# Optimization experiments

Measured on AMD Instinct MI355X. Metric: run time of the kernel, lower is better.

The kernel has to match this reference:

```python
import jax, jax.numpy as jnp
import numpy as np

N_FFT = 1024
HOP_LENGTH = 480
NB_MAX_FRAMES = 1000
N_MELS = 64
SPEC_WIDTH = 1024
N_BINS = N_FFT // 2 + 1  # 513


def setup_inputs() -> dict:
    key = jax.random.key(0)
    B, L = 32, 480000  # 10 s @ 48 kHz -> 1001 frames, truncated to 1000
    waveform = jax.random.normal(key, (B, L), dtype=jnp.float32)

    # DFT-as-conv weights, exactly as in the torch module (hann periodic window)
    n = np.arange(N_FFT, dtype=np.float32)
    window = 0.5 - 0.5 * np.cos(2.0 * np.pi * n / N_FFT)  # torch.hann_window (periodic)
    k = np.arange(N_BINS, dtype=np.float32)[:, None]
    angle = 2.0 * np.pi * k * n[None, :] / N_FFT
    stft_weights = np.concatenate(
        [window * np.cos(angle), -window * np.sin(angle)], axis=0
    ).astype(np.float32)  # [2*N_BINS, N_FFT]

    # Stand-in for HF's slaney mel filterbank (513 -> 64): non-negative, sparse-ish scale
    mel_filters = jax.random.uniform(
        jax.random.fold_in(key, 1), (N_BINS, N_MELS), dtype=jnp.float32
    ) * 0.02

    return {
        "waveform": waveform,
        "stft_weights": jnp.asarray(stft_weights),
        "mel_filters": mel_filters,
    }


def _bilinear_align_corners(img, out_h, out_w):
    """F.interpolate(mode='bilinear', align_corners=True) on [B,C,H,W]."""
    B, C, H, W = img.shape

    def coords(out, inn):
        scale = (inn - 1) / max(out - 1, 1)
        pos = jnp.arange(out, dtype=jnp.float32) * scale
        i0 = jnp.clip(jnp.floor(pos).astype(jnp.int32), 0, inn - 1)
        return i0, pos - i0.astype(jnp.float32)

    h0, hw = coords(out_h, H)
    w0, ww = coords(out_w, W)
    h1 = jnp.minimum(h0 + 1, H - 1)
    w1 = jnp.minimum(w0 + 1, W - 1)

    rows = (img[:, :, h0, :] * (1.0 - hw)[None, None, :, None]
            + img[:, :, h1, :] * hw[None, None, :, None])  # [B,C,out_h,W]
    out = rows[..., w0] * (1.0 - ww) + rows[..., w1] * ww   # [B,C,out_h,out_w]
    return out


def reference(waveform, stft_weights, mel_filters):
    pad = N_FFT // 2
    x = jnp.pad(waveform, ((0, 0), (pad, pad)), mode="reflect")  # center=True

    # strided conv1d == frame extraction + GEMM with the DFT matrix
    T = (x.shape[1] - N_FFT) // HOP_LENGTH + 1
    idx = jnp.arange(T)[:, None] * HOP_LENGTH + jnp.arange(N_FFT)[None, :]
    frames = x[:, idx]                                   # [B, T, N_FFT]
    spec = jnp.einsum("btn,kn->bkt", frames, stft_weights)  # [B, 2*N_BINS, T]

    real = spec[:, :N_BINS, :]
    imag = spec[:, N_BINS:, :]
    power = (real * real + imag * imag)[:, :, :NB_MAX_FRAMES]  # [B, 513, 1000]

    mel = jnp.einsum("bft,fm->bmt", power, mel_filters)        # [B, 64, 1000]
    log_mel = 10.0 * jnp.log10(jnp.clip(mel, 1e-10))

    img = jnp.transpose(log_mel, (0, 2, 1))[:, None]           # [B, 1, 1000, 64]
    return _bilinear_align_corners(img, SPEC_WIDTH, N_MELS)    # [B, 1, 1024, 64]
```

## Files before the change

kernel.cpp:

```cpp
#include <hip/hip_runtime.h>
#include <hip/hip_bf16.h>
#include <math.h>

#define LWAV   480000
#define XHALF  240512
#define NBATCH 32
#define TOUT   1000
#define NMEL   64
#define PSTR   576
#define SPECW  1024

#define XPE_OFF  0u
#define XPO_OFF  15392768u
#define WEO_OFF  30785536u
#define WMT_OFF  31834112u
#define PW_OFF   31907840u
#define LM_OFF   68771840u
#define W256_OFF 76963840u

typedef __attribute__((ext_vector_type(8))) __bf16 bf16x8;
typedef __attribute__((ext_vector_type(8))) unsigned short ushort8;
typedef __attribute__((ext_vector_type(4))) float  f32x4;

__device__ __forceinline__ void gload16(const void* g, void* l) {
  __builtin_amdgcn_global_load_lds((const __attribute__((address_space(1))) void*)g,
                                   (__attribute__((address_space(3))) void*)l, 16, 0, 0);
}
#define WAIT_VM(n)  asm volatile("s_waitcnt vmcnt(" #n ")" ::: "memory")
#define BAR() __builtin_amdgcn_s_barrier()

__device__ __forceinline__ float bf2f(unsigned short u) {
  return __uint_as_float((unsigned)u << 16);
}

#define NG1 (NBATCH * (XHALF / 8))
#define NG2 ((1024 * 512) / 8)
#define NG3 ((NMEL * PSTR) / 8)
#define NG4 (1024 / 8)

__global__ void prep_kernel(const float* __restrict__ wav,
                            const float* __restrict__ wstft,
                            const float* __restrict__ mf,
                            unsigned char* __restrict__ ws) {
  __hip_bfloat16* xpE = (__hip_bfloat16*)(ws + XPE_OFF);
  __hip_bfloat16* xpO = (__hip_bfloat16*)(ws + XPO_OFF);
  __hip_bfloat16* weo = (__hip_bfloat16*)(ws + WEO_OFF);
  __hip_bfloat16* wmt = (__hip_bfloat16*)(ws + WMT_OFF);
  __hip_bfloat16* w256 = (__hip_bfloat16*)(ws + W256_OFF);
  int idx = blockIdx.x * blockDim.x + threadIdx.x;
  if (idx < NG1) {
    int b = idx / (XHALF / 8);
    int g = idx - b * (XHALF / 8);
    const float* src = wav + (size_t)b * LWAV;
    __hip_bfloat16 e[8], o[8];
    if (g >= 32 && g <= 30030) {
      const float4* p = (const float4*)(src + 16 * g - 512);
#pragma unroll
      for (int u = 0; u < 4; ++u) {
        float4 v = p[u];
        e[2 * u]     = __float2bfloat16(v.x);
        o[2 * u]     = __float2bfloat16(v.y);
        e[2 * u + 1] = __float2bfloat16(v.z);
        o[2 * u + 1] = __float2bfloat16(v.w);
      }
    } else {
      for (int i = 0; i < 16; ++i) {
        int q = 16 * g + i;
        int s = q - 512;
        if (s < 0) s = -s;
        else if (s >= LWAV) s = 2 * (LWAV - 1) - s;
        __hip_bfloat16 v = __float2bfloat16(src[s]);
        if (i & 1) o[i >> 1] = v; else e[i >> 1] = v;
      }
    }
    *(uint4*)(xpE + (size_t)b * XHALF + 8 * g) = *(const uint4*)e;
    *(uint4*)(xpO + (size_t)b * XHALF + 8 * g) = *(const uint4*)o;
  } else if (idx < NG1 + NG2) {
    int v = idx - NG1;
    int row = v >> 6;
    int mseg = (v & 63) * 8;
    int comp = row >> 8, j = row & 255;
    __hip_bfloat16 t[8];
    if (comp < 2) {
      const float4* srow = (const float4*)(wstft + (size_t)(comp == 0 ? j : 513 + j) * 1024 + 2 * mseg);
#pragma unroll
      for (int u = 0; u < 4; ++u) {
        float4 vv = srow[u];
        t[2 * u]     = __float2bfloat16(vv.x);
        t[2 * u + 1] = __float2bfloat16(vv.z);
      }
    } else {
      const float4* w0 = (const float4*)(wstft + 2 * mseg);
#pragma unroll
      for (int u = 0; u < 4; ++u) {
        float4 wwv = w0[u];
        float wo[2] = {wwv.y, wwv.w};
#pragma unroll
        for (int h = 0; h < 2; ++h) {
          int mm = mseg + 2 * u + h;
          int q = (j * mm) & 511;
          float ang = (float)q * 0.012271846f;
          float val = (comp == 2) ? wo[h] * cosf(ang) : -wo[h] * sinf(ang);
          t[2 * u + h] = __float2bfloat16(val);
        }
      }
    }
    *(uint4*)(weo + (size_t)row * 512 + mseg) = *(const uint4*)t;
  } else if (idx < NG1 + NG2 + NG3) {
    int j = idx - NG1 - NG2;
    int n = j / (PSTR / 8);
    int k0 = (j - n * (PSTR / 8)) * 8;
    for (int k = k0; k < k0 + 8; ++k)
      wmt[n * PSTR + k] = __float2bfloat16(k < 513 ? mf[k * NMEL + n] : 0.0f);
  } else if (idx < NG1 + NG2 + NG3 + NG4) {
    int j = idx - NG1 - NG2 - NG3;
    int part = j >> 6;
    int m0 = (j & 63) * 8;
    __hip_bfloat16 t[8];
#pragma unroll
    for (int h = 0; h < 8; ++h) {
      int m = m0 + h;
      float v = part == 0 ? wstft[(size_t)256 * 1024 + 2 * m]
                          : wstft[(size_t)769 * 1024 + 2 * m + 1];
      t[h] = __float2bfloat16(v);
    }
    *(uint4*)(w256 + part * 512 + m0) = *(const uint4*)t;
  }
}

__launch_bounds__(256, 2)
__global__ void p256_kernel(unsigned char* __restrict__ ws) {
  __hip_bfloat16* pw = (__hip_bfloat16*)(ws + PW_OFF);
  const int tid  = threadIdx.x;
  const int l16  = tid & 15;
  const int fidx = blockIdx.x * 16 + (tid >> 4);
  const int b = fidx / 1000, t = fidx - b * 1000;

  const unsigned short* xe = (const unsigned short*)(ws + XPE_OFF) +
      (size_t)b * XHALF + 240 * (size_t)t + l16 * 32;
  const unsigned short* xo = (const unsigned short*)(ws + XPO_OFF) +
      (size_t)b * XHALF + 240 * (size_t)t + l16 * 32;
  const unsigned short* we = (const unsigned short*)(ws + W256_OFF) + l16 * 32;
  const unsigned short* wo = (const unsigned short*)(ws + W256_OFF) + 512 + l16 * 32;

  ushort8 ev[4], ov[4], wev[4], wov[4];
#pragma unroll
  for (int q = 0; q < 4; ++q) {
    ev[q]  = *(const ushort8*)(xe + q * 8);
    ov[q]  = *(const ushort8*)(xo + q * 8);
    wev[q] = *(const ushort8*)(we + q * 8);
    wov[q] = *(const ushort8*)(wo + q * 8);
  }
  float dc = 0.f, ds = 0.f;
#pragma unroll
  for (int q = 0; q < 4; ++q)
#pragma unroll
    for (int u = 0; u < 8; ++u) {
      dc += bf2f(ev[q][u]) * bf2f(wev[q][u]);
      ds += bf2f(ov[q][u]) * bf2f(wov[q][u]);
    }
#pragma unroll
  for (int d = 1; d < 16; d <<= 1) {
    dc += __shfl_xor(dc, d);
    ds += __shfl_xor(ds, d);
  }
  if (l16 == 0)
    pw[((size_t)b * TOUT + t) * PSTR + 256] = __float2bfloat16(dc * dc + ds * ds);
}

#define STFT_NWG 500
__launch_bounds__(512, 1)
__global__ void stft_kernel(unsigned char* __restrict__ ws) {
  __shared__ __align__(16) unsigned char lds[147456];
  __hip_bfloat16* pw = (__hip_bfloat16*)(ws + PW_OFF);

  const int tid  = threadIdx.x;
  const int lane = tid & 63;
  const int w    = tid >> 6;
  const int wm   = w >> 2;
  const int wc   = w & 3;

  const int orig = blockIdx.x;
  const int q8 = STFT_NWG / 8, r8 = STFT_NWG % 8;
  const int xcd = orig & 7;
  const int wg = (xcd < r8 ? xcd * (q8 + 1) : r8 * (q8 + 1) + (xcd - r8) * q8) + (orig >> 3);
  const int j0 = (wg & 3) * 64;
  const int m0 = (wg >> 2) * 256;

  const unsigned char* gsA[4];
  const unsigned char* gsB[2];
#pragma unroll
  for (int i = 0; i < 4; ++i) {
    int r = (w * 4 + i) * 8 + (lane >> 3);
    int q = lane & 7;
    int l1 = q ^ (r & 7);
    int m = m0 + r;
    int bb = m / 1000, tt = m - bb * 1000;
    size_t fbase = ((size_t)bb * XHALF + 240 * (size_t)tt) * 2;
    gsA[i] = (l1 < 4) ? (ws + XPE_OFF + fbase + l1 * 16)
                      : (ws + XPO_OFF + fbase + (l1 - 4) * 16);
  }
#pragma unroll
  for (int i = 0; i < 2; ++i) {
    int r = (w * 2 + i) * 16 + (lane >> 2);
    int q = lane & 3;
    int l2 = q ^ ((r >> 1) & 3);
    int comp = (r >> 4) & 3;
    int jv = j0 + (r >> 6) * 16 + (r & 15);
    gsB[i] = ws + WEO_OFF + ((size_t)(comp * 256 + jv) * 512) * 2 + l2 * 16;
  }

#define STG(c, kt) do {                                                          \
    gload16(gsA[0] + (size_t)(kt) * 64, lds + (c) * 49152 + (w * 4 + 0) * 1024); \
    gload16(gsA[1] + (size_t)(kt) * 64, lds + (c) * 49152 + (w * 4 + 1) * 1024); \
    gload16(gsA[2] + (size_t)(kt) * 64, lds + (c) * 49152 + (w * 4 + 2) * 1024); \
    gload16(gsA[3] + (size_t)(kt) * 64, lds + (c) * 49152 + (w * 4 + 3) * 1024); \
    gload16(gsB[0] + (size_t)(kt) * 64, lds + (c) * 49152 + 32768 + (w * 2 + 0) * 1024); \
    gload16(gsB[1] + (size_t)(kt) * 64, lds + (c) * 49152 + 32768 + (w * 2 + 1) * 1024); \
  } while (0)

  const int l15 = lane & 15, lc = lane >> 4;
  const int swA = (lc ^ (l15 & 7)) << 4;
  const unsigned char* aeB = lds + (wm * 128 + l15) * 128 + swA;
  const unsigned char* aoB = lds + (wm * 128 + l15) * 128 + (swA ^ 64);
  const int swB = (lc ^ ((l15 >> 1) & 3)) << 4;
  const unsigned char* bB = lds + 32768 + (wc * 64 + l15) * 64 + swB;

  bf16x8 ae[8], ao[8], bfr[4];
  f32x4 acc[8][4];
#pragma unroll
  for (int a = 0; a < 8; ++a)
#pragma unroll
    for (int b2 = 0; b2 < 4; ++b2) acc[a][b2] = (f32x4){0.f, 0.f, 0.f, 0.f};

  STG(0, 0);
  STG(1, 1);
  WAIT_VM(6);
  BAR();

#pragma unroll
  for (int kt = 0; kt < 16; ++kt) {
    const int cur = kt % 3;
    if (kt + 2 < 16) STG((kt + 2) % 3, kt + 2);
#pragma unroll
    for (int mf = 0; mf < 8; ++mf)
      ae[mf] = *(const bf16x8*)(aeB + cur * 49152 + mf * 2048);
#pragma unroll
    for (int nf = 0; nf < 4; ++nf)
      bfr[nf] = *(const bf16x8*)(bB + cur * 49152 + nf * 1024);
    __builtin_amdgcn_s_setprio(1);
#pragma unroll
    for (int mf = 0; mf < 8; ++mf) {
      acc[mf][0] = __builtin_amdgcn_mfma_f32_16x16x32_bf16(ae[mf], bfr[0], acc[mf][0], 0, 0, 0);
      acc[mf][1] = __builtin_amdgcn_mfma_f32_16x16x32_bf16(ae[mf], bfr[1], acc[mf][1], 0, 0, 0);
    }
    __builtin_amdgcn_s_setprio(0);
#pragma unroll
    for (int mf = 0; mf < 8; ++mf)
      ao[mf] = *(const bf16x8*)(aoB + cur * 49152 + mf * 2048);
    __builtin_amdgcn_s_setprio(1);
#pragma unroll
    for (int mf = 0; mf < 8; ++mf) {
      acc[mf][2] = __builtin_amdgcn_mfma_f32_16x16x32_bf16(ao[mf], bfr[2], acc[mf][2], 0, 0, 0);
      acc[mf][3] = __builtin_amdgcn_mfma_f32_16x16x32_bf16(ao[mf], bfr[3], acc[mf][3], 0, 0, 0);
    }
    __builtin_amdgcn_s_setprio(0);
    if (kt < 14) { WAIT_VM(6); BAR(); }
    else if (kt == 14) { WAIT_VM(0); BAR(); }
  }

  const int j = j0 + wc * 16 + l15;
  const float th = (float)j * 0.0061359233f;
  const float ct = cosf(th), st = sinf(th);
#pragma unroll
  for (int mf = 0; mf < 8; ++mf)
#pragma unroll
    for (int r = 0; r < 4; ++r) {
      int m = m0 + wm * 128 + mf * 16 + lc * 4 + r;
      float Ec = acc[mf][0][r], Es = acc[mf][1][r];
      float Oc = acc[mf][2][r], Os = acc[mf][3][r];
      float tOc = ct * Oc + st * Os;
      float tOs = ct * Os - st * Oc;
      float re1 = Ec + tOc, im1 = Es + tOs;
      float re2 = Ec - tOc, im2 = Es - tOs;
      pw[(size_t)m * PSTR + j]         = __float2bfloat16(re1 * re1 + im1 * im1);
      pw[(size_t)m * PSTR + (512 - j)] = __float2bfloat16(re2 * re2 + im2 * im2);
    }
}

__launch_bounds__(256, 4)
__global__ void mel_kernel(unsigned char* __restrict__ ws) {
  __shared__ __align__(16) unsigned char sA[64 * 128];
  __shared__ __align__(16) unsigned char sBt[64 * 128];
  const unsigned char* pwb  = ws + PW_OFF;
  const unsigned char* wmtb = ws + WMT_OFF;
  float* lm = (float*)(ws + LM_OFF);

  const int tid = threadIdx.x;
  const int lane = tid & 63;
  const int wid  = tid >> 6;
  const int m0 = blockIdx.x * 64;

  const int strow = tid >> 3;
  const int scol  = (tid & 7) << 4;

  const unsigned char* aptr[2];
  const unsigned char* bptr[2];
  unsigned char* aldst[2];
  unsigned char* bldst[2];
#pragma unroll
  for (int jj = 0; jj < 2; ++jj) {
    int rr = jj * 32 + strow;
    aptr[jj] = pwb + (size_t)(m0 + rr) * (PSTR * 2) + (scol ^ ((rr & 7) << 4));
    bptr[jj] = wmtb + (size_t)rr * (PSTR * 2) + (scol ^ ((rr & 7) << 4));
    aldst[jj] = &sA [jj * 4096 + wid * 1024];
    bldst[jj] = &sBt[jj * 4096 + wid * 1024];
  }

  f32x4 acc[4];
#pragma unroll
  for (int fr = 0; fr < 4; ++fr) acc[fr] = (f32x4){0.f, 0.f, 0.f, 0.f};

  for (int kk = 0; kk < PSTR; kk += 64) {
    __syncthreads();
#pragma unroll
    for (int jj = 0; jj < 2; ++jj) gload16(aptr[jj] + (size_t)kk * 2, aldst[jj]);
#pragma unroll
    for (int jj = 0; jj < 2; ++jj) gload16(bptr[jj] + (size_t)kk * 2, bldst[jj]);
    __syncthreads();
#pragma unroll
    for (int ks = 0; ks < 2; ++ks) {
      const int kby = ks * 64 + ((lane >> 4) << 4);
      bf16x8 af, bfr[4];
      {
        int rr = wid * 16 + (lane & 15);
        af = *(const bf16x8*)&sA[rr * 128 + (kby ^ ((rr & 7) << 4))];
      }
#pragma unroll
      for (int fr = 0; fr < 4; ++fr) {
        int rr = fr * 16 + (lane & 15);
        bfr[fr] = *(const bf16x8*)&sBt[rr * 128 + (kby ^ ((rr & 7) << 4))];
      }
#pragma unroll
      for (int fr = 0; fr < 4; ++fr)
        acc[fr] = __builtin_amdgcn_mfma_f32_16x16x32_bf16(af, bfr[fr], acc[fr], 0, 0, 0);
    }
  }

  const int col = lane & 15;
  const int rg  = lane >> 4;
#pragma unroll
  for (int fr = 0; fr < 4; ++fr) {
    int n = fr * 16 + col;
#pragma unroll
    for (int rr = 0; rr < 4; ++rr) {
      int mrow = wid * 16 + rg * 4 + rr;
      float v = acc[fr][rr];
      lm[(size_t)(m0 + mrow) * NMEL + n] = 10.0f * log10f(fmaxf(v, 1e-10f));
    }
  }
}

__global__ void interp_kernel(const unsigned char* __restrict__ ws, float* __restrict__ out) {
  const float* lm = (const float*)(ws + LM_OFF);
  int idx = blockIdx.x * blockDim.x + threadIdx.x;
  if (idx >= NBATCH * SPECW * 16) return;
  int m4 = idx & 15;
  int h  = (idx >> 4) & (SPECW - 1);
  int b  = idx >> 14;
  const float scale = (float)(999.0 / 1023.0);
  float pos = (float)h * scale;
  int i0 = (int)floorf(pos);
  if (i0 > TOUT - 1) i0 = TOUT - 1;
  float wgt = pos - (float)i0;
  int i1 = i0 + 1;
  if (i1 > TOUT - 1) i1 = TOUT - 1;
  const float4* r0 = (const float4*)(lm + ((size_t)b * TOUT + i0) * NMEL);
  const float4* r1 = (const float4*)(lm + ((size_t)b * TOUT + i1) * NMEL);
  float4 a = r0[m4], c = r1[m4];
  float4 o;
  o.x = a.x * (1.0f - wgt) + c.x * wgt;
  o.y = a.y * (1.0f - wgt) + c.y * wgt;
  o.z = a.z * (1.0f - wgt) + c.z * wgt;
  o.w = a.w * (1.0f - wgt) + c.w * wgt;
  ((float4*)out)[idx] = o;
}

extern "C" void kernel_launch(void* const* d_in, const int* in_sizes, int n_in,
                              void* d_out, int out_size, void* d_ws, size_t ws_size,
                              hipStream_t stream) {
  (void)in_sizes; (void)n_in; (void)out_size; (void)ws_size;
  const float* wav   = (const float*)d_in[0];
  const float* wstft = (const float*)d_in[1];
  const float* mf    = (const float*)d_in[2];
  unsigned char* ws  = (unsigned char*)d_ws;
  float* out = (float*)d_out;

  const int tot = NG1 + NG2 + NG3 + NG4;
  prep_kernel<<<(tot + 255) / 256, 256, 0, stream>>>(wav, wstft, mf, ws);
  stft_kernel<<<STFT_NWG, 512, 0, stream>>>(ws);
  p256_kernel<<<2000, 256, 0, stream>>>(ws);
  mel_kernel<<<500, 256, 0, stream>>>(ws);
  interp_kernel<<<(NBATCH * SPECW * 16) / 256, 256, 0, stream>>>(ws, out);
}
```

Before: 90.69 us.

## Retile STFT GEMM to 128x256 blocks with double buffering and two blocks per CU

```diff
diff --git a/kernel.cpp b/kernel.cpp
--- a/kernel.cpp
+++ b/kernel.cpp
@@ -27,6 +27,7 @@
                                    (__attribute__((address_space(3))) void*)l, 16, 0, 0);
 }
 #define WAIT_VM(n)  asm volatile("s_waitcnt vmcnt(" #n ")" ::: "memory")
+#define WAIT_LGKM0  asm volatile("s_waitcnt lgkmcnt(0)" ::: "memory")
 #define BAR() __builtin_amdgcn_s_barrier()
 
 __device__ __forceinline__ float bf2f(unsigned short u) {
@@ -168,124 +169,141 @@
     pw[((size_t)b * TOUT + t) * PSTR + 256] = __float2bfloat16(dc * dc + ds * ds);
 }
 
-#define STFT_NWG 500
-__launch_bounds__(512, 1)
+#define STFT_NWG 1000
+__launch_bounds__(256, 2)
 __global__ void stft_kernel(unsigned char* __restrict__ ws) {
-  __shared__ __align__(16) unsigned char lds[147456];
+  __shared__ __align__(16) unsigned char lds[65536];
   __hip_bfloat16* pw = (__hip_bfloat16*)(ws + PW_OFF);
 
   const int tid  = threadIdx.x;
   const int lane = tid & 63;
   const int w    = tid >> 6;
-  const int wm   = w >> 2;
-  const int wc   = w & 3;
+  const int wm   = w >> 1;
+  const int wn   = w & 1;
 
   const int orig = blockIdx.x;
-  const int q8 = STFT_NWG / 8, r8 = STFT_NWG % 8;
-  const int xcd = orig & 7;
-  const int wg = (xcd < r8 ? xcd * (q8 + 1) : r8 * (q8 + 1) + (xcd - r8) * q8) + (orig >> 3);
+  const int wg = (orig & 7) * 125 + (orig >> 3);
   const int j0 = (wg & 3) * 64;
-  const int m0 = (wg >> 2) * 256;
+  const int m0 = (wg >> 2) * 128;
 
   const unsigned char* gsA[4];
-  const unsigned char* gsB[2];
-#pragma unroll
-  for (int i = 0; i < 4; ++i) {
-    int r = (w * 4 + i) * 8 + (lane >> 3);
-    int q = lane & 7;
-    int l1 = q ^ (r & 7);
-    int m = m0 + r;
-    int bb = m / 1000, tt = m - bb * 1000;
-    size_t fbase = ((size_t)bb * XHALF + 240 * (size_t)tt) * 2;
-    gsA[i] = (l1 < 4) ? (ws + XPE_OFF + fbase + l1 * 16)
-                      : (ws + XPO_OFF + fbase + (l1 - 4) * 16);
-  }
-#pragma unroll
-  for (int i = 0; i < 2; ++i) {
-    int r = (w * 2 + i) * 16 + (lane >> 2);
-    int q = lane & 3;
-    int l2 = q ^ ((r >> 1) & 3);
-    int comp = (r >> 4) & 3;
-    int jv = j0 + (r >> 6) * 16 + (r & 15);
-    gsB[i] = ws + WEO_OFF + ((size_t)(comp * 256 + jv) * 512) * 2 + l2 * 16;
-  }
-
-#define STG(c, kt) do {                                                          \
-    gload16(gsA[0] + (size_t)(kt) * 64, lds + (c) * 49152 + (w * 4 + 0) * 1024); \
-    gload16(gsA[1] + (size_t)(kt) * 64, lds + (c) * 49152 + (w * 4 + 1) * 1024); \
-    gload16(gsA[2] + (size_t)(kt) * 64, lds + (c) * 49152 + (w * 4 + 2) * 1024); \
-    gload16(gsA[3] + (size_t)(kt) * 64, lds + (c) * 49152 + (w * 4 + 3) * 1024); \
-    gload16(gsB[0] + (size_t)(kt) * 64, lds + (c) * 49152 + 32768 + (w * 2 + 0) * 1024); \
-    gload16(gsB[1] + (size_t)(kt) * 64, lds + (c) * 49152 + 32768 + (w * 2 + 1) * 1024); \
+  {
+    int sl  = tid & 7;
+    int rq  = tid >> 3;
+    int slp = sl ^ (rq & 7);
+#pragma unroll
+    for (int i = 0; i < 4; ++i) {
+      int row = i * 32 + rq;
+      int m = m0 + row;
+      int bb = m / 1000, tt = m - bb * 1000;
+      size_t fb = ((size_t)bb * XHALF + 240 * (size_t)tt) * 2;
+      gsA[i] = (slp < 4) ? (ws + XPE_OFF + fb + slp * 16)
+                         : (ws + XPO_OFF + fb + (slp - 4) * 16);
+    }
+  }
+  const unsigned char* gsB[4];
+  {
+    int sl2  = tid & 3;
+    int rq2  = tid >> 2;
+    int sl2p = sl2 ^ (rq2 & 3);
+#pragma unroll
+    for (int i = 0; i < 4; ++i) {
+      int row2 = i * 64 + rq2;
+      int comp = (row2 >> 4) & 3;
+      int jj = j0 + (row2 >> 6) * 16 + (row2 & 15);
+      gsB[i] = ws + WEO_OFF + (size_t)(comp * 256 + jj) * 1024 + sl2p * 16;
+    }
+  }
+
+#define STG(c, kt) do {                                                           \
+    gload16(gsA[0] + (size_t)(kt) * 64, lds + (c) * 32768 + 0 * 4096 + w * 1024); \
+    gload16(gsA[1] + (size_t)(kt) * 64, lds + (c) * 32768 + 1 * 4096 + w * 1024); \
+    gload16(gsA[2] + (size_t)(kt) * 64, lds + (c) * 32768 + 2 * 4096 + w * 1024); \
+    gload16(gsA[3] + (size_t)(kt) * 64, lds + (c) * 32768 + 3 * 4096 + w * 1024); \
+    gload16(gsB[0] + (size_t)(kt) * 64, lds + (c) * 32768 + 16384 + 0 * 4096 + w * 1024); \
+    gload16(gsB[1] + (size_t)(kt) * 64, lds + (c) * 32768 + 16384 + 1 * 4096 + w * 1024); \
+    gload16(gsB[2] + (size_t)(kt) * 64, lds + (c) * 32768 + 16384 + 2 * 4096 + w * 1024); \
+    gload16(gsB[3] + (size_t)(kt) * 64, lds + (c) * 32768 + 16384 + 3 * 4096 + w * 1024); \
   } while (0)
 
   const int l15 = lane & 15, lc = lane >> 4;
-  const int swA = (lc ^ (l15 & 7)) << 4;
-  const unsigned char* aeB = lds + (wm * 128 + l15) * 128 + swA;
-  const unsigned char* aoB = lds + (wm * 128 + l15) * 128 + (swA ^ 64);
-  const int swB = (lc ^ ((l15 >> 1) & 3)) << 4;
-  const unsigned char* bB = lds + 32768 + (wc * 64 + l15) * 64 + swB;
-
-  bf16x8 ae[8], ao[8], bfr[4];
-  f32x4 acc[8][4];
-#pragma unroll
-  for (int a = 0; a < 8; ++a)
-#pragma unroll
-    for (int b2 = 0; b2 < 4; ++b2) acc[a][b2] = (f32x4){0.f, 0.f, 0.f, 0.f};
+  const int aoffs = (wm * 64 + l15) * 128 + ((lc ^ (l15 & 7)) << 4);
+  const int boffs = 16384 + (wn * 128 + l15) * 64 + ((lc ^ (l15 & 3)) << 4);
+
+  bf16x8 ae[4], ao[4], bfr[8];
+  f32x4 acc[4][8];
+#pragma unroll
+  for (int a = 0; a < 4; ++a)
+#pragma unroll
+    for (int b2 = 0; b2 < 8; ++b2) acc[a][b2] = (f32x4){0.f, 0.f, 0.f, 0.f};
+
+#define RD_ALL(C) do {                                                       \
+    _Pragma("unroll")                                                        \
+    for (int mf = 0; mf < 4; ++mf) {                                         \
+      ae[mf] = *(const bf16x8*)(lds + (C) + aoffs + mf * 2048);              \
+      ao[mf] = *(const bf16x8*)(lds + (C) + (aoffs ^ 64) + mf * 2048);       \
+    }                                                                        \
+    _Pragma("unroll")                                                        \
+    for (int nf = 0; nf < 8; ++nf)                                           \
+      bfr[nf] = *(const bf16x8*)(lds + (C) + boffs + nf * 1024);             \
+  } while (0)
+
+#define MFMA_ALL() do {                                                      \
+    __builtin_amdgcn_s_setprio(1);                                           \
+    _Pragma("unroll")                                                        \
+    for (int mf = 0; mf < 4; ++mf)                                           \
+      _Pragma("unroll")                                                      \
+      for (int g = 0; g < 2; ++g) {                                          \
+        acc[mf][g*4+0] = __builtin_amdgcn_mfma_f32_16x16x32_bf16(            \
+            ae[mf], bfr[g*4+0], acc[mf][g*4+0], 0, 0, 0);                    \
+        acc[mf][g*4+1] = __builtin_amdgcn_mfma_f32_16x16x32_bf16(            \
+            ae[mf], bfr[g*4+1], acc[mf][g*4+1], 0, 0, 0);                    \
+        acc[mf][g*4+2] = __builtin_amdgcn_mfma_f32_16x16x32_bf16(            \
+            ao[mf], bfr[g*4+2], acc[mf][g*4+2], 0, 0, 0);                    \
+        acc[mf][g*4+3] = __builtin_amdgcn_mfma_f32_16x16x32_bf16(            \
+            ao[mf], bfr[g*4+3], acc[mf][g*4+3], 0, 0, 0);                    \
+      }                                                                      \
+    __builtin_amdgcn_s_setprio(0);                                           \
+  } while (0)
 
   STG(0, 0);
   STG(1, 1);
-  WAIT_VM(6);
+  WAIT_VM(8);
   BAR();
 
 #pragma unroll
   for (int kt = 0; kt < 16; ++kt) {
-    const int cur = kt % 3;
-    if (kt + 2 < 16) STG((kt + 2) % 3, kt + 2);
-#pragma unroll
-    for (int mf = 0; mf < 8; ++mf)
-      ae[mf] = *(const bf16x8*)(aeB + cur * 49152 + mf * 2048);
-#pragma unroll
-    for (int nf = 0; nf < 4; ++nf)
-      bfr[nf] = *(const bf16x8*)(bB + cur * 49152 + nf * 1024);
-    __builtin_amdgcn_s_setprio(1);
-#pragma unroll
-    for (int mf = 0; mf < 8; ++mf) {
-      acc[mf][0] = __builtin_amdgcn_mfma_f32_16x16x32_bf16(ae[mf], bfr[0], acc[mf][0], 0, 0, 0);
-      acc[mf][1] = __builtin_amdgcn_mfma_f32_16x16x32_bf16(ae[mf], bfr[1], acc[mf][1], 0, 0, 0);
-    }
-    __builtin_amdgcn_s_setprio(0);
-#pragma unroll
-    for (int mf = 0; mf < 8; ++mf)
-      ao[mf] = *(const bf16x8*)(aoB + cur * 49152 + mf * 2048);
-    __builtin_amdgcn_s_setprio(1);
-#pragma unroll
-    for (int mf = 0; mf < 8; ++mf) {
-      acc[mf][2] = __builtin_amdgcn_mfma_f32_16x16x32_bf16(ao[mf], bfr[2], acc[mf][2], 0, 0, 0);
-      acc[mf][3] = __builtin_amdgcn_mfma_f32_16x16x32_bf16(ao[mf], bfr[3], acc[mf][3], 0, 0, 0);
-    }
-    __builtin_amdgcn_s_setprio(0);
-    if (kt < 14) { WAIT_VM(6); BAR(); }
-    else if (kt == 14) { WAIT_VM(0); BAR(); }
-  }
-
-  const int j = j0 + wc * 16 + l15;
-  const float th = (float)j * 0.0061359233f;
-  const float ct = cosf(th), st = sinf(th);
-#pragma unroll
-  for (int mf = 0; mf < 8; ++mf)
-#pragma unroll
-    for (int r = 0; r < 4; ++r) {
-      int m = m0 + wm * 128 + mf * 16 + lc * 4 + r;
-      float Ec = acc[mf][0][r], Es = acc[mf][1][r];
-      float Oc = acc[mf][2][r], Os = acc[mf][3][r];
-      float tOc = ct * Oc + st * Os;
-      float tOs = ct * Os - st * Oc;
-      float re1 = Ec + tOc, im1 = Es + tOs;
-      float re2 = Ec - tOc, im2 = Es - tOs;
-      pw[(size_t)m * PSTR + j]         = __float2bfloat16(re1 * re1 + im1 * im1);
-      pw[(size_t)m * PSTR + (512 - j)] = __float2bfloat16(re2 * re2 + im2 * im2);
-    }
+    const int c = kt & 1;
+    RD_ALL(c * 32768);
+    MFMA_ALL();
+    if (kt == 15) break;
+    WAIT_LGKM0;
+    BAR();
+    if (kt + 2 < 16) STG(c, kt + 2);
+    if (kt < 14) { WAIT_VM(8); } else { WAIT_VM(0); }
+    BAR();
+  }
+
+#pragma unroll
+  for (int g = 0; g < 2; ++g) {
+    int j = j0 + wn * 32 + g * 16 + l15;
+    float th = (float)j * 0.0061359233f;
+    float ct = cosf(th), st = sinf(th);
+#pragma unroll
+    for (int mf = 0; mf < 4; ++mf)
+#pragma unroll
+      for (int r = 0; r < 4; ++r) {
+        int m = m0 + wm * 64 + mf * 16 + lc * 4 + r;
+        float Ec = acc[mf][g*4+0][r], Es = acc[mf][g*4+1][r];
+        float Oc = acc[mf][g*4+2][r], Os = acc[mf][g*4+3][r];
+        float tOc = ct * Oc + st * Os;
+        float tOs = ct * Os - st * Oc;
+        float re1 = Ec + tOc, im1 = Es + tOs;
+        float re2 = Ec - tOc, im2 = Es - tOs;
+        pw[(size_t)m * PSTR + j]         = __float2bfloat16(re1 * re1 + im1 * im1);
+        pw[(size_t)m * PSTR + (512 - j)] = __float2bfloat16(re2 * re2 + im2 * im2);
+      }
+  }
 }
 
 __launch_bounds__(256, 4)
@@ -398,7 +416,7 @@
 
   const int tot = NG1 + NG2 + NG3 + NG4;
   prep_kernel<<<(tot + 255) / 256, 256, 0, stream>>>(wav, wstft, mf, ws);
-  stft_kernel<<<STFT_NWG, 512, 0, stream>>>(ws);
+  stft_kernel<<<STFT_NWG, 256, 0, stream>>>(ws);
   p256_kernel<<<2000, 256, 0, stream>>>(ws);
   mel_kernel<<<500, 256, 0, stream>>>(ws);
   interp_kernel<<<(NBATCH * SPECW * 16) / 256, 256, 0, stream>>>(ws, out);
```

After: 93.91 us. 1.04x slower.
